# Kernel optimization log

Hardware: AMD Instinct MI355X
Metric: run time of the kernel (lower is better)

Reference implementation:

```python
import jax, jax.numpy as jnp
import numpy as np

B, S, D = 4, 1024, 1024
H, DK, DV = 16, 64, 64


def setup_inputs() -> dict:
    key = jax.random.key(0)
    ks = jax.random.split(key, 8)
    sc = 0.02
    return {
        "queries": jax.random.normal(ks[0], (B, S, D), jnp.float32),
        "keys": jax.random.normal(ks[1], (B, S, D), jnp.float32),
        "values": jax.random.normal(ks[2], (B, S, D), jnp.float32),
        "attn_bias": jax.random.normal(ks[3], (B, 1, S, S), jnp.float32),
        "Wq": jax.random.normal(ks[4], (H * DK, D), jnp.float32) * sc,
        "Wk": jax.random.normal(ks[5], (H * DK, D), jnp.float32) * sc,
        "Wv": jax.random.normal(ks[6], (H * DV, D), jnp.float32) * sc,
        "Wp": jax.random.normal(ks[7], (D, H * DV), jnp.float32) * sc,
    }


def reference(queries, keys, values, attn_bias, Wq, Wk, Wv, Wp):
    # Linear (no bias): x @ W.T, then split heads -> [B, H, S, d]
    q = (queries @ Wq.T).reshape(B, S, H, DK).transpose(0, 2, 1, 3)
    k = (keys @ Wk.T).reshape(B, S, H, DK).transpose(0, 2, 1, 3)
    v = (values @ Wv.T).reshape(B, S, H, DV).transpose(0, 2, 1, 3)
    # NOTE: original scales by d_model**-0.5, not d_key**-0.5
    scores = jnp.einsum("bhqd,bhkd->bhqk", q, k) * (D ** -0.5)
    scores = scores + attn_bias  # bias broadcasts over heads
    weights = jax.nn.softmax(scores, axis=-1)
    out = jnp.einsum("bhqk,bhkd->bhqd", weights, v)  # [B,H,S,DV]
    out = out.transpose(0, 2, 1, 3).reshape(B, S, H * DV)
    return out @ Wp.T
```

## Files before the change

### kernel.cpp

```cpp
#include <hip/hip_runtime.h>
#include <hip/hip_bf16.h>

typedef unsigned short u16;
typedef unsigned int u32;
typedef __attribute__((ext_vector_type(8))) short bf16x8;
typedef __attribute__((ext_vector_type(8))) u16 u16x8;
typedef __attribute__((ext_vector_type(4))) u16 u16x4;
typedef __attribute__((ext_vector_type(4))) u32 u32x4;
typedef __attribute__((ext_vector_type(4))) float f32x4;
typedef __attribute__((ext_vector_type(4))) _Float16 f16x4;
typedef __attribute__((ext_vector_type(8))) _Float16 f16x8;
typedef __attribute__((ext_vector_type(16))) float f32x16;

typedef const __attribute__((address_space(1))) void* gas1_t;
typedef __attribute__((address_space(3))) void* las3_t;

#define MFMA16(a,b,c) __builtin_amdgcn_mfma_f32_16x16x32_bf16((a),(b),(c),0,0,0)
#define MFMA32(a,b,c) __builtin_amdgcn_mfma_f32_32x32x16_bf16((a),(b),(c),0,0,0)

static constexpr int BB = 4, SS = 1024, DD = 1024, HH = 16;

static __device__ __forceinline__ u16 f2b(float x) {
  union { __hip_bfloat16 h; u16 u; } cv;
  cv.h = __float2bfloat16(x);
  return cv.u;
}
static __device__ __forceinline__ u32 pk2(float a, float b) {
  return (u32)f2b(a) | ((u32)f2b(b) << 16);
}

__global__ __launch_bounds__(256) void cvt_all(
    const float* __restrict__ q, const float* __restrict__ k, const float* __restrict__ v,
    const float* __restrict__ wq_, const float* __restrict__ wk_, const float* __restrict__ wv_,
    const float* __restrict__ wp_, const float* __restrict__ bias,
    u16* __restrict__ qb, u16* __restrict__ kb, u16* __restrict__ vb,
    u16* __restrict__ wqb, u16* __restrict__ wkb, u16* __restrict__ wvb, u16* __restrict__ wpb,
    _Float16* __restrict__ bias16) {
  int bid = blockIdx.x;
  if (bid >= 16384) {
    int G = (bid - 16384) * 256 + threadIdx.x;
    int gi = G & 1023;
    int ctid = gi & 255, g = gi >> 8;
    int T = G >> 10;
    int kt = T & 15, qt = (T >> 4) & 7, b_ = T >> 7;
    int wq = ctid >> 6, hi = (ctid >> 5) & 1, ln = ctid & 31;
    int qrow = qt * 128 + wq * 32 + ln;
    int kbf = g >> 1, j = g & 1;
    int k0 = kt * 64 + kbf * 32 + j * 16 + hi * 4;
    const float* src = bias + (((size_t)(b_ * 1024 + qrow)) << 10) + k0;
    float4 lo = *(const float4*)(src);
    float4 up = *(const float4*)(src + 8);
    f16x8 r = { (_Float16)lo.x, (_Float16)lo.y, (_Float16)lo.z, (_Float16)lo.w,
                (_Float16)up.x, (_Float16)up.y, (_Float16)up.z, (_Float16)up.w };
    *(f16x8*)(bias16 + (((size_t)T) << 13) + g * 2048 + ctid * 8) = r;
    return;
  }
  const float* s; u16* d; int off;
  if      (bid < 4096)  { s = q;   d = qb;  off = bid; }
  else if (bid < 8192)  { s = k;   d = kb;  off = bid - 4096; }
  else if (bid < 12288) { s = v;   d = vb;  off = bid - 8192; }
  else if (bid < 13312) { s = wq_; d = wqb; off = bid - 12288; }
  else if (bid < 14336) { s = wk_; d = wkb; off = bid - 13312; }
  else if (bid < 15360) { s = wv_; d = wvb; off = bid - 14336; }
  else                  { s = wp_; d = wpb; off = bid - 15360; }
  int i = (off * 256 + threadIdx.x) * 4;
  float4 val = *(const float4*)(s + i);
  u16x4 r = { f2b(val.x), f2b(val.y), f2b(val.z), f2b(val.w) };
  *(u16x4*)(d + i) = r;
}

template<typename OT, bool VTRANS>
__global__ __launch_bounds__(256) void gemm_bt(
    const u16* __restrict__ Abase, const u16* __restrict__ Wbase, OT* __restrict__ Cbase,
    u16* __restrict__ Tout, int N, int K, size_t sA, size_t sW, size_t sC) {
  const u16* A = Abase + (size_t)blockIdx.z * sA;
  const u16* W = Wbase + (size_t)blockIdx.z * sW;
  OT* C = Cbase + (size_t)blockIdx.z * sC;

  __shared__ __align__(16) u16 As[128 * 64];
  __shared__ __align__(16) u16 Bs[128 * 64];

  const int tid = threadIdx.x;
  const int lane = tid & 63;
  const int wid = tid >> 6;
  const int g = lane >> 4;
  const int li = lane & 15;

  const int hw = blockIdx.x + (blockIdx.y << 3);
  const int L = ((hw & 7) << 5) + (hw >> 3);
  const int brow = (L >> 3) * 128;
  const int bcol = (L & 7) * 128;

  const int wr = (wid >> 1) * 64;
  const int wc = (wid & 1) * 64;

  const int srow = wid * 8 + (lane >> 3);
  const int schunk = (lane & 7) ^ (lane >> 3);
  const u16* ga0 = A + (size_t)(brow + srow) * K + schunk * 8;
  const u16* gw0 = W + (size_t)(bcol + srow) * K + schunk * 8;

  f32x4 acc[4][4] = {};

  for (int k0 = 0; k0 < K; k0 += 64) {
#pragma unroll
    for (int i = 0; i < 4; ++i) {
      __builtin_amdgcn_global_load_lds((gas1_t)(const void*)(ga0 + (size_t)(i * 32) * K + k0),
                                       (las3_t)(void*)(As + (i * 32 + wid * 8) * 64), 16, 0, 0);
      __builtin_amdgcn_global_load_lds((gas1_t)(const void*)(gw0 + (size_t)(i * 32) * K + k0),
                                       (las3_t)(void*)(Bs + (i * 32 + wid * 8) * 64), 16, 0, 0);
    }
    __syncthreads();

#pragma unroll
    for (int kk = 0; kk < 2; ++kk) {
      bf16x8 a[4], b[4];
#pragma unroll
      for (int m = 0; m < 4; ++m) {
        int row = wr + m * 16 + li;
        a[m] = *(const bf16x8*)&As[row * 64 + (((kk * 4 + g) ^ (li & 7)) << 3)];
      }
#pragma unroll
      for (int n = 0; n < 4; ++n) {
        int row = wc + n * 16 + li;
        b[n] = *(const bf16x8*)&Bs[row * 64 + (((kk * 4 + g) ^ (li & 7)) << 3)];
      }
#pragma unroll
      for (int m = 0; m < 4; ++m)
#pragma unroll
        for (int n = 0; n < 4; ++n)
          acc[m][n] = MFMA16(a[m], b[n], acc[m][n]);
    }
    __syncthreads();
  }

  if (VTRANS && blockIdx.z == 2) {
#pragma unroll
    for (int m = 0; m < 4; ++m) {
#pragma unroll
      for (int n = 0; n < 4; ++n) {
        int c = bcol + wc + n * 16 + li;
        int h_ = c >> 6, dv = c & 63;
        int r0 = brow + wr + m * 16 + g * 4;
        int b_ = r0 >> 10, s0 = r0 & 1023;
        u16x4 val = { f2b(acc[m][n][0]), f2b(acc[m][n][1]),
                      f2b(acc[m][n][2]), f2b(acc[m][n][3]) };
        *(u16x4*)&Tout[(size_t)((b_ * HH + h_) * 64 + dv) * SS + s0] = val;
      }
    }
  } else {
#pragma unroll
    for (int m = 0; m < 4; ++m)
#pragma unroll
      for (int n = 0; n < 4; ++n)
#pragma unroll
        for (int j = 0; j < 4; ++j) {
          int r = brow + wr + m * 16 + g * 4 + j;
          int c = bcol + wc + n * 16 + li;
          if constexpr (sizeof(OT) == 2) C[(size_t)r * N + c] = (OT)f2b(acc[m][n][j]);
          else                           C[(size_t)r * N + c] = acc[m][n][j];
        }
  }
}

__global__ __launch_bounds__(512) void gemm_proj(
    const u16* __restrict__ A, const u16* __restrict__ W, float* __restrict__ C,
    int N, int K) {
  __shared__ __align__(16) u16 As[128 * 64];
  __shared__ __align__(16) u16 Bs[128 * 64];

  const int tid = threadIdx.x;
  const int lane = tid & 63;
  const int wid = tid >> 6;
  const int g = lane >> 4;
  const int li = lane & 15;

  const int hw = blockIdx.x + (blockIdx.y << 3);
  const int L = ((hw & 7) << 5) + (hw >> 3);
  const int brow = (L >> 3) * 128;
  const int bcol = (L & 7) * 128;

  const int wr = (wid >> 1) * 32;
  const int wc = (wid & 1) * 64;

  const int srow = tid >> 3;
  const int schunk = (tid & 7) ^ (srow & 7);
  const u16* ga0 = A + (size_t)(brow + srow) * K + schunk * 8;
  const u16* gw0 = W + (size_t)(bcol + srow) * K + schunk * 8;

  f32x4 acc[2][4] = {};

  for (int k0 = 0; k0 < K; k0 += 64) {
#pragma unroll
    for (int i = 0; i < 2; ++i) {
      __builtin_amdgcn_global_load_lds((gas1_t)(const void*)(ga0 + (size_t)(i * 64) * K + k0),
                                       (las3_t)(void*)(As + (i * 64 + (wid << 3)) * 64), 16, 0, 0);
      __builtin_amdgcn_global_load_lds((gas1_t)(const void*)(gw0 + (size_t)(i * 64) * K + k0),
                                       (las3_t)(void*)(Bs + (i * 64 + (wid << 3)) * 64), 16, 0, 0);
    }
    __syncthreads();

#pragma unroll
    for (int kk = 0; kk < 2; ++kk) {
      bf16x8 a[2], b[4];
#pragma unroll
      for (int m = 0; m < 2; ++m) {
        int row = wr + m * 16 + li;
        a[m] = *(const bf16x8*)&As[row * 64 + (((kk * 4 + g) ^ (li & 7)) << 3)];
      }
#pragma unroll
      for (int n = 0; n < 4; ++n) {
        int row = wc + n * 16 + li;
        b[n] = *(const bf16x8*)&Bs[row * 64 + (((kk * 4 + g) ^ (li & 7)) << 3)];
      }
#pragma unroll
      for (int m = 0; m < 2; ++m)
#pragma unroll
        for (int n = 0; n < 4; ++n)
          acc[m][n] = MFMA16(a[m], b[n], acc[m][n]);
    }
    __syncthreads();
  }

#pragma unroll
  for (int m = 0; m < 2; ++m)
#pragma unroll
    for (int n = 0; n < 4; ++n)
#pragma unroll
      for (int j = 0; j < 4; ++j) {
        int r = brow + wr + m * 16 + g * 4 + j;
        int c = bcol + wc + n * 16 + li;
        C[(size_t)r * N + c] = acc[m][n][j];
      }
}

__global__ __launch_bounds__(256) void attn_kernel(
    const u16* __restrict__ Q, const u16* __restrict__ K, const u16* __restrict__ Vt,
    const _Float16* __restrict__ bias16, u16* __restrict__ O) {
  __shared__ __align__(16) u16 kbuf[2][64 * 64];
  __shared__ __align__(16) u16 vbuf[2][64 * 64];

  const int tid = threadIdx.x;
  const int lane = tid & 63;
  const int wq = tid >> 6;
  const int hi = lane >> 5;
  const int ln = lane & 31;
  const u32 swz = (u32)(ln & 7) << 4;

  const int flat = blockIdx.x + (blockIdx.y << 3) + (blockIdx.z << 7);
  const int L = ((flat & 7) << 6) | (flat >> 3);
  const int qt = L & 7, h = (L >> 3) & 15, b = L >> 7;
  const int q0 = qt * 128;
  const int qrow = q0 + wq * 32 + ln;

  bf16x8 qf[4];
  {
    const u16* qp = Q + (size_t)(b * SS + qrow) * DD + h * 64 + hi * 8;
#pragma unroll
    for (int d = 0; d < 4; ++d) qf[d] = *(const bf16x8*)(qp + d * 16);
  }

  const int srow = (lane >> 3);
  const int spc = ((lane & 7) ^ srow) * 8;
  const u16* kgl = K + (size_t)(b * SS + wq * 16 + srow) * DD + h * 64 + spc;
  const u16* vgl = Vt + (size_t)((b * HH + h) * 64 + wq * 16 + srow) * SS + spc;

  const _Float16* btile = bias16 + (((size_t)(b * 8 + qt) * 16) << 13) + tid * 8;

  {
    char* kd = (char*)kbuf[0] + wq * 2048;
    char* vd = (char*)vbuf[0] + wq * 2048;
#pragma unroll
    for (int j = 0; j < 2; ++j) {
      __builtin_amdgcn_global_load_lds((gas1_t)(const void*)(kgl + (size_t)(j * 8) * DD),
                                       (las3_t)(void*)(kd + j * 1024), 16, 0, 0);
      __builtin_amdgcn_global_load_lds((gas1_t)(const void*)(vgl + (size_t)(j * 8) * SS),
                                       (las3_t)(void*)(vd + j * 1024), 16, 0, 0);
    }
  }
  f16x8 bbr[4], bbn[4];
#pragma unroll
  for (int g = 0; g < 4; ++g)
    bbr[g] = *(const f16x8*)(btile + g * 2048);
  __syncthreads();

  f32x16 o0 = {}, o1 = {};
  float m = -1e30f, lsum = 0.f;
  int cur = 0;

  for (int kt = 0; kt < 16; ++kt) {
    if (kt < 15) {
      char* kd = (char*)kbuf[cur ^ 1] + wq * 2048;
      char* vd = (char*)vbuf[cur ^ 1] + wq * 2048;
      const size_t k1 = (size_t)(kt + 1) * 64;
#pragma unroll
      for (int j = 0; j < 2; ++j) {
        __builtin_amdgcn_global_load_lds((gas1_t)(const void*)(kgl + (k1 + j * 8) * DD),
                                         (las3_t)(void*)(kd + j * 1024), 16, 0, 0);
        __builtin_amdgcn_global_load_lds((gas1_t)(const void*)(vgl + (size_t)(j * 8) * SS + k1),
                                         (las3_t)(void*)(vd + j * 1024), 16, 0, 0);
      }
      const _Float16* bt = btile + ((size_t)(kt + 1) << 13);
#pragma unroll
      for (int g = 0; g < 4; ++g)
        bbn[g] = *(const f16x8*)(bt + g * 2048);
    }

    const char* kb_base = (const char*)kbuf[cur];
    f32x16 s[2];
#pragma unroll
    for (int kb = 0; kb < 2; ++kb) {
      f32x16 acc = {};
#pragma unroll
      for (int d = 0; d < 4; ++d) {
        bf16x8 kf = *(const bf16x8*)(kb_base + (kb * 32 + ln) * 128 + (((u32)(d * 32 + hi * 16)) ^ swz));
        acc = MFMA32(kf, qf[d], acc);
      }
      s[kb] = acc;
    }

#pragma unroll
    for (int g = 0; g < 4; ++g) {
      const int kb = g >> 1, rq0 = (g & 1) * 2;
#pragma unroll
      for (int e = 0; e < 8; ++e)
        s[kb][(rq0 + (e >> 2)) * 4 + (e & 3)] =
            fmaf(s[kb][(rq0 + (e >> 2)) * 4 + (e & 3)], 0.03125f, (float)bbr[g][e]);
    }

    float mt = -1e30f;
#pragma unroll
    for (int r = 0; r < 16; ++r) { mt = fmaxf(mt, s[0][r]); mt = fmaxf(mt, s[1][r]); }
    mt = fmaxf(mt, __shfl_xor(mt, 32));

    bool resc = false;
    float fsc = 1.f;
    if (kt == 0) {
      m = mt;
    } else if (__any(mt > m + 8.f)) {
      float mn = fmaxf(m, mt);
      fsc = __expf(m - mn);
      m = mn;
      resc = true;
    }

    float rs = 0.f;
    u32 wv[2][8];
#pragma unroll
    for (int kb = 0; kb < 2; ++kb)
#pragma unroll
      for (int t = 0; t < 8; ++t) {
        float p0 = __expf(s[kb][2 * t] - m);
        float p1 = __expf(s[kb][2 * t + 1] - m);
        rs += p0 + p1;
        wv[kb][t] = pk2(p0, p1);
      }
    rs += __shfl_xor(rs, 32);
    lsum = lsum * fsc + rs;

    if (resc) {
#pragma unroll
      for (int j = 0; j < 16; ++j) {
        float fv = __shfl(fsc, (j & 3) + 8 * (j >> 2) + 4 * hi);
        o0[j] *= fv; o1[j] *= fv;
      }
    }

    const char* vb_base = (const char*)vbuf[cur];
#pragma unroll
    for (int ks = 0; ks < 4; ++ks) {
      const int kb = ks >> 1, i0 = (ks & 1) * 4;
      u32 sA = hi ? wv[kb][i0 + 0] : wv[kb][i0 + 2];
      u32 sB = hi ? wv[kb][i0 + 1] : wv[kb][i0 + 3];
      u32 rA = (u32)__shfl_xor((int)sA, 32);
      u32 rB = (u32)__shfl_xor((int)sB, 32);
      u32 e0 = hi ? rA : wv[kb][i0 + 0];
      u32 e1 = hi ? rB : wv[kb][i0 + 1];
      u32 e2 = hi ? wv[kb][i0 + 2] : rA;
      u32 e3 = hi ? wv[kb][i0 + 3] : rB;
      union { u32x4 u; bf16x8 v; } pc;
      pc.u = (u32x4){e0, e1, e2, e3};
      bf16x8 pa = pc.v;
#pragma unroll
      for (int nv = 0; nv < 2; ++nv) {
        bf16x8 vf = *(const bf16x8*)(vb_base + (nv * 32 + ln) * 128 + (((u32)(ks * 32 + hi * 16)) ^ swz));
        if (nv == 0) o0 = MFMA32(pa, vf, o0);
        else         o1 = MFMA32(pa, vf, o1);
      }
    }

    if (kt < 15) {
      __syncthreads();
      cur ^= 1;
#pragma unroll
      for (int g = 0; g < 4; ++g) bbr[g] = bbn[g];
    }
  }

  float inv = 1.0f / lsum;
#pragma unroll
  for (int j = 0; j < 16; ++j) {
    float iv = __shfl(inv, (j & 3) + 8 * (j >> 2) + 4 * hi);
    int q = q0 + wq * 32 + (j & 3) + 8 * (j >> 2) + 4 * hi;
    u16* op = O + (size_t)(b * SS + q) * DD + h * 64 + ln;
    op[0]  = f2b(o0[j] * iv);
    op[32] = f2b(o1[j] * iv);
  }
}

extern "C" void kernel_launch(void* const* d_in, const int* in_sizes, int n_in,
                              void* d_out, int out_size, void* d_ws, size_t ws_size,
                              hipStream_t stream) {
  const float* queries = (const float*)d_in[0];
  const float* keys    = (const float*)d_in[1];
  const float* values  = (const float*)d_in[2];
  const float* bias    = (const float*)d_in[3];
  const float* Wq      = (const float*)d_in[4];
  const float* Wk      = (const float*)d_in[5];
  const float* Wv      = (const float*)d_in[6];
  const float* Wp      = (const float*)d_in[7];
  float* out = (float*)d_out;

  char* ws = (char*)d_ws;
  const size_t MB = 1024 * 1024;
  u16* qb  = (u16*)(ws + 0 * MB);
  u16* kb  = (u16*)(ws + 8 * MB);
  u16* vb  = (u16*)(ws + 16 * MB);
  u16* wqb = (u16*)(ws + 24 * MB);
  u16* wkb = (u16*)(ws + 26 * MB);
  u16* wvb = (u16*)(ws + 28 * MB);
  u16* wpb = (u16*)(ws + 30 * MB);
  u16* Qb  = (u16*)(ws + 32 * MB);
  u16* Kb  = (u16*)(ws + 40 * MB);
  _Float16* bias16 = (_Float16*)(ws + 48 * MB);
  u16* Vtb = (u16*)(ws + 56 * MB);
  u16* Ob  = (u16*)(ws + 0 * MB);

  const int nAct = BB * SS * DD;
  const int nW = DD * DD;

  cvt_all<<<dim3(18432), dim3(256), 0, stream>>>(
      queries, keys, values, Wq, Wk, Wv, Wp, bias,
      qb, kb, vb, wqb, wkb, wvb, wpb, bias16);

  gemm_bt<u16, true><<<dim3(8, 32, 3), dim3(256), 0, stream>>>(
      qb, wqb, Qb, Vtb, DD, DD, (size_t)nAct, (size_t)nW, (size_t)nAct);

  attn_kernel<<<dim3(8, 16, 4), dim3(256), 0, stream>>>(Qb, Kb, Vtb, bias16, Ob);

  gemm_proj<<<dim3(8, 32), dim3(512), 0, stream>>>(Ob, wpb, out, DD, DD);
}
```

Measured before the change: 117.4 us.

## Double the attention key tile to 128 and load bias at iteration start

Result: slower. 125.8 us (+7.1%).

```diff
diff --git a/kernel.cpp b/kernel.cpp
--- a/kernel.cpp
+++ b/kernel.cpp
@@ -236,15 +236,16 @@
 __global__ __launch_bounds__(256) void attn_kernel(
     const u16* __restrict__ Q, const u16* __restrict__ K, const u16* __restrict__ Vt,
     const _Float16* __restrict__ bias16, u16* __restrict__ O) {
-  __shared__ __align__(16) u16 kbuf[2][64 * 64];
-  __shared__ __align__(16) u16 vbuf[2][64 * 64];
+  __shared__ __align__(16) u16 kbuf[2][128 * 64];
+  __shared__ __align__(16) u16 vbuf[2][64 * 128];
 
   const int tid = threadIdx.x;
   const int lane = tid & 63;
   const int wq = tid >> 6;
   const int hi = lane >> 5;
   const int ln = lane & 31;
-  const u32 swz = (u32)(ln & 7) << 4;
+  const u32 swzK = (u32)(ln & 7) << 4;
+  const u32 swzV = (u32)(ln & 15) << 4;
 
   const int flat = blockIdx.x + (blockIdx.y << 3) + (blockIdx.z << 7);
   const int L = ((flat & 7) << 6) | (flat >> 3);
@@ -259,77 +260,79 @@
     for (int d = 0; d < 4; ++d) qf[d] = *(const bf16x8*)(qp + d * 16);
   }
 
-  const int srow = (lane >> 3);
-  const int spc = ((lane & 7) ^ srow) * 8;
-  const u16* kgl = K + (size_t)(b * SS + wq * 16 + srow) * DD + h * 64 + spc;
-  const u16* vgl = Vt + (size_t)((b * HH + h) * 64 + wq * 16 + srow) * SS + spc;
+  const int sr8 = lane >> 3;
+  const int spcK = ((lane & 7) ^ sr8) * 8;
+  const u16* kgl = K + (size_t)(b * SS + wq * 32 + sr8) * DD + h * 64 + spcK;
+
+  const int vr4 = lane >> 4;
+  const u16* vgl = Vt + (size_t)((b * HH + h) * 64 + wq * 16 + vr4) * SS;
 
   const _Float16* btile = bias16 + (((size_t)(b * 8 + qt) * 16) << 13) + tid * 8;
 
-  {
-    char* kd = (char*)kbuf[0] + wq * 2048;
-    char* vd = (char*)vbuf[0] + wq * 2048;
-#pragma unroll
-    for (int j = 0; j < 2; ++j) {
-      __builtin_amdgcn_global_load_lds((gas1_t)(const void*)(kgl + (size_t)(j * 8) * DD),
-                                       (las3_t)(void*)(kd + j * 1024), 16, 0, 0);
-      __builtin_amdgcn_global_load_lds((gas1_t)(const void*)(vgl + (size_t)(j * 8) * SS),
-                                       (las3_t)(void*)(vd + j * 1024), 16, 0, 0);
-    }
-  }
-  f16x8 bbr[4], bbn[4];
-#pragma unroll
-  for (int g = 0; g < 4; ++g)
-    bbr[g] = *(const f16x8*)(btile + g * 2048);
+#define STAGE_KV(buf, ktv)                                                                 \
+  {                                                                                        \
+    char* kd = (char*)kbuf[buf] + wq * 4096;                                               \
+    char* vd = (char*)vbuf[buf] + wq * 4096;                                               \
+    _Pragma("unroll")                                                                      \
+    for (int j = 0; j < 4; ++j)                                                            \
+      __builtin_amdgcn_global_load_lds(                                                    \
+          (gas1_t)(const void*)(kgl + (size_t)((ktv) * 128 + j * 8) * DD),                 \
+          (las3_t)(void*)(kd + j * 1024), 16, 0, 0);                                       \
+    _Pragma("unroll")                                                                      \
+    for (int j = 0; j < 4; ++j)                                                            \
+      __builtin_amdgcn_global_load_lds(                                                    \
+          (gas1_t)(const void*)(vgl + (size_t)(j * 4) * SS + (ktv) * 128 +                 \
+                                ((lane & 15) ^ (j * 4 + vr4)) * 8),                        \
+          (las3_t)(void*)(vd + j * 1024), 16, 0, 0);                                       \
+  }
+
+  STAGE_KV(0, 0)
   __syncthreads();
 
   f32x16 o0 = {}, o1 = {};
   float m = -1e30f, lsum = 0.f;
   int cur = 0;
 
-  for (int kt = 0; kt < 16; ++kt) {
-    if (kt < 15) {
-      char* kd = (char*)kbuf[cur ^ 1] + wq * 2048;
-      char* vd = (char*)vbuf[cur ^ 1] + wq * 2048;
-      const size_t k1 = (size_t)(kt + 1) * 64;
-#pragma unroll
-      for (int j = 0; j < 2; ++j) {
-        __builtin_amdgcn_global_load_lds((gas1_t)(const void*)(kgl + (k1 + j * 8) * DD),
-                                         (las3_t)(void*)(kd + j * 1024), 16, 0, 0);
-        __builtin_amdgcn_global_load_lds((gas1_t)(const void*)(vgl + (size_t)(j * 8) * SS + k1),
-                                         (las3_t)(void*)(vd + j * 1024), 16, 0, 0);
-      }
-      const _Float16* bt = btile + ((size_t)(kt + 1) << 13);
-#pragma unroll
-      for (int g = 0; g < 4; ++g)
-        bbn[g] = *(const f16x8*)(bt + g * 2048);
-    }
+  for (int kt = 0; kt < 8; ++kt) {
+    f16x8 bbr[8];
+    {
+      const _Float16* bt = btile + ((size_t)(kt * 2) << 13);
+#pragma unroll
+      for (int g = 0; g < 4; ++g) bbr[g] = *(const f16x8*)(bt + g * 2048);
+#pragma unroll
+      for (int g = 0; g < 4; ++g) bbr[4 + g] = *(const f16x8*)(bt + 8192 + g * 2048);
+    }
+    if (kt < 7) STAGE_KV(cur ^ 1, kt + 1)
 
     const char* kb_base = (const char*)kbuf[cur];
-    f32x16 s[2];
-#pragma unroll
-    for (int kb = 0; kb < 2; ++kb) {
+    f32x16 s[4];
+#pragma unroll
+    for (int kbf = 0; kbf < 4; ++kbf) {
       f32x16 acc = {};
 #pragma unroll
       for (int d = 0; d < 4; ++d) {
-        bf16x8 kf = *(const bf16x8*)(kb_base + (kb * 32 + ln) * 128 + (((u32)(d * 32 + hi * 16)) ^ swz));
+        bf16x8 kf = *(const bf16x8*)(kb_base + (kbf * 32 + ln) * 128 + (((u32)(d * 32 + hi * 16)) ^ swzK));
         acc = MFMA32(kf, qf[d], acc);
       }
-      s[kb] = acc;
-    }
-
-#pragma unroll
-    for (int g = 0; g < 4; ++g) {
-      const int kb = g >> 1, rq0 = (g & 1) * 2;
+      s[kbf] = acc;
+    }
+
+#pragma unroll
+    for (int gp = 0; gp < 8; ++gp) {
+      const int kbf = ((gp >> 2) << 1) | ((gp >> 1) & 1), rq0 = (gp & 1) * 2;
 #pragma unroll
       for (int e = 0; e < 8; ++e)
-        s[kb][(rq0 + (e >> 2)) * 4 + (e & 3)] =
-            fmaf(s[kb][(rq0 + (e >> 2)) * 4 + (e & 3)], 0.03125f, (float)bbr[g][e]);
-    }
-
-    float mt = -1e30f;
-#pragma unroll
-    for (int r = 0; r < 16; ++r) { mt = fmaxf(mt, s[0][r]); mt = fmaxf(mt, s[1][r]); }
+        s[kbf][(rq0 + (e >> 2)) * 4 + (e & 3)] =
+            fmaf(s[kbf][(rq0 + (e >> 2)) * 4 + (e & 3)], 0.03125f, (float)bbr[gp][e]);
+    }
+
+    float r16[16];
+#pragma unroll
+    for (int i = 0; i < 16; ++i)
+      r16[i] = fmaxf(fmaxf(s[0][i], s[1][i]), fmaxf(s[2][i], s[3][i]));
+    float mt = r16[0];
+#pragma unroll
+    for (int i = 1; i < 16; ++i) mt = fmaxf(mt, r16[i]);
     mt = fmaxf(mt, __shfl_xor(mt, 32));
 
     bool resc = false;
@@ -344,15 +347,15 @@
     }
 
     float rs = 0.f;
-    u32 wv[2][8];
-#pragma unroll
-    for (int kb = 0; kb < 2; ++kb)
+    u32 wv[4][8];
+#pragma unroll
+    for (int kbf = 0; kbf < 4; ++kbf)
 #pragma unroll
       for (int t = 0; t < 8; ++t) {
-        float p0 = __expf(s[kb][2 * t] - m);
-        float p1 = __expf(s[kb][2 * t + 1] - m);
+        float p0 = __expf(s[kbf][2 * t] - m);
+        float p1 = __expf(s[kbf][2 * t + 1] - m);
         rs += p0 + p1;
-        wv[kb][t] = pk2(p0, p1);
+        wv[kbf][t] = pk2(p0, p1);
       }
     rs += __shfl_xor(rs, 32);
     lsum = lsum * fsc + rs;
@@ -367,34 +370,33 @@
 
     const char* vb_base = (const char*)vbuf[cur];
 #pragma unroll
-    for (int ks = 0; ks < 4; ++ks) {
-      const int kb = ks >> 1, i0 = (ks & 1) * 4;
-      u32 sA = hi ? wv[kb][i0 + 0] : wv[kb][i0 + 2];
-      u32 sB = hi ? wv[kb][i0 + 1] : wv[kb][i0 + 3];
+    for (int ks = 0; ks < 8; ++ks) {
+      const int kbf = ks >> 1, i0 = (ks & 1) * 4;
+      u32 sA = hi ? wv[kbf][i0 + 0] : wv[kbf][i0 + 2];
+      u32 sB = hi ? wv[kbf][i0 + 1] : wv[kbf][i0 + 3];
       u32 rA = (u32)__shfl_xor((int)sA, 32);
       u32 rB = (u32)__shfl_xor((int)sB, 32);
-      u32 e0 = hi ? rA : wv[kb][i0 + 0];
-      u32 e1 = hi ? rB : wv[kb][i0 + 1];
-      u32 e2 = hi ? wv[kb][i0 + 2] : rA;
-      u32 e3 = hi ? wv[kb][i0 + 3] : rB;
+      u32 e0 = hi ? rA : wv[kbf][i0 + 0];
+      u32 e1 = hi ? rB : wv[kbf][i0 + 1];
+      u32 e2 = hi ? wv[kbf][i0 + 2] : rA;
+      u32 e3 = hi ? wv[kbf][i0 + 3] : rB;
       union { u32x4 u; bf16x8 v; } pc;
       pc.u = (u32x4){e0, e1, e2, e3};
       bf16x8 pa = pc.v;
 #pragma unroll
       for (int nv = 0; nv < 2; ++nv) {
-        bf16x8 vf = *(const bf16x8*)(vb_base + (nv * 32 + ln) * 128 + (((u32)(ks * 32 + hi * 16)) ^ swz));
+        bf16x8 vf = *(const bf16x8*)(vb_base + (nv * 32 + ln) * 256 + (((u32)(ks * 32 + hi * 16)) ^ swzV));
         if (nv == 0) o0 = MFMA32(pa, vf, o0);
         else         o1 = MFMA32(pa, vf, o1);
       }
     }
 
-    if (kt < 15) {
+    if (kt < 7) {
       __syncthreads();
       cur ^= 1;
-#pragma unroll
-      for (int g = 0; g < 4; ++g) bbr[g] = bbn[g];
-    }
-  }
+    }
+  }
+#undef STAGE_KV
 
   float inv = 1.0f / lsum;
 #pragma unroll
```

## Fuse fp32-to-bf16 activation conversion into QKV projection GEMM

Applied to the files above, without the earlier changes.

Measured after the change: 112.4 us. -4.3%, faster.

```diff
diff --git a/kernel.cpp b/kernel.cpp
--- a/kernel.cpp
+++ b/kernel.cpp
@@ -28,17 +28,20 @@
 static __device__ __forceinline__ u32 pk2(float a, float b) {
   return (u32)f2b(a) | ((u32)f2b(b) << 16);
 }
+static __device__ __forceinline__ u32 cvtpk(float lo, float hi) {
+  u32 r;
+  asm("v_cvt_pk_bf16_f32 %0, %1, %2" : "=v"(r) : "v"(lo), "v"(hi));
+  return r;
+}
 
 __global__ __launch_bounds__(256) void cvt_all(
-    const float* __restrict__ q, const float* __restrict__ k, const float* __restrict__ v,
     const float* __restrict__ wq_, const float* __restrict__ wk_, const float* __restrict__ wv_,
     const float* __restrict__ wp_, const float* __restrict__ bias,
-    u16* __restrict__ qb, u16* __restrict__ kb, u16* __restrict__ vb,
     u16* __restrict__ wqb, u16* __restrict__ wkb, u16* __restrict__ wvb, u16* __restrict__ wpb,
     _Float16* __restrict__ bias16) {
   int bid = blockIdx.x;
-  if (bid >= 16384) {
-    int G = (bid - 16384) * 256 + threadIdx.x;
+  if (bid >= 4096) {
+    int G = (bid - 4096) * 256 + threadIdx.x;
     int gi = G & 1023;
     int ctid = gi & 255, g = gi >> 8;
     int T = G >> 10;
@@ -56,28 +59,25 @@
     return;
   }
   const float* s; u16* d; int off;
-  if      (bid < 4096)  { s = q;   d = qb;  off = bid; }
-  else if (bid < 8192)  { s = k;   d = kb;  off = bid - 4096; }
-  else if (bid < 12288) { s = v;   d = vb;  off = bid - 8192; }
-  else if (bid < 13312) { s = wq_; d = wqb; off = bid - 12288; }
-  else if (bid < 14336) { s = wk_; d = wkb; off = bid - 13312; }
-  else if (bid < 15360) { s = wv_; d = wvb; off = bid - 14336; }
-  else                  { s = wp_; d = wpb; off = bid - 15360; }
+  if      (bid < 1024) { s = wq_; d = wqb; off = bid; }
+  else if (bid < 2048) { s = wk_; d = wkb; off = bid - 1024; }
+  else if (bid < 3072) { s = wv_; d = wvb; off = bid - 2048; }
+  else                 { s = wp_; d = wpb; off = bid - 3072; }
   int i = (off * 256 + threadIdx.x) * 4;
   float4 val = *(const float4*)(s + i);
   u16x4 r = { f2b(val.x), f2b(val.y), f2b(val.z), f2b(val.w) };
   *(u16x4*)(d + i) = r;
 }
 
-template<typename OT, bool VTRANS>
-__global__ __launch_bounds__(256) void gemm_bt(
-    const u16* __restrict__ Abase, const u16* __restrict__ Wbase, OT* __restrict__ Cbase,
-    u16* __restrict__ Tout, int N, int K, size_t sA, size_t sW, size_t sC) {
-  const u16* A = Abase + (size_t)blockIdx.z * sA;
-  const u16* W = Wbase + (size_t)blockIdx.z * sW;
-  OT* C = Cbase + (size_t)blockIdx.z * sC;
-
-  __shared__ __align__(16) u16 As[128 * 64];
+__global__ __launch_bounds__(512) void gemm_qkv(
+    const float* __restrict__ Qf, const float* __restrict__ Kf, const float* __restrict__ Vf,
+    const u16* __restrict__ Wbase, u16* __restrict__ Qb, u16* __restrict__ Kb,
+    u16* __restrict__ Vtb) {
+  const int z = blockIdx.z;
+  const float* A = z == 0 ? Qf : (z == 1 ? Kf : Vf);
+  const u16* W = Wbase + (size_t)z * (DD * DD);
+
+  __shared__ __align__(16) float Af[128 * 64];
   __shared__ __align__(16) u16 Bs[128 * 64];
 
   const int tid = threadIdx.x;
@@ -91,33 +91,43 @@
   const int brow = (L >> 3) * 128;
   const int bcol = (L & 7) * 128;
 
-  const int wr = (wid >> 1) * 64;
+  const int wr = (wid >> 1) * 32;
   const int wc = (wid & 1) * 64;
 
-  const int srow = wid * 8 + (lane >> 3);
-  const int schunk = (lane & 7) ^ (lane >> 3);
-  const u16* ga0 = A + (size_t)(brow + srow) * K + schunk * 8;
-  const u16* gw0 = W + (size_t)(bcol + srow) * K + schunk * 8;
-
-  f32x4 acc[4][4] = {};
-
-  for (int k0 = 0; k0 < K; k0 += 64) {
-#pragma unroll
-    for (int i = 0; i < 4; ++i) {
-      __builtin_amdgcn_global_load_lds((gas1_t)(const void*)(ga0 + (size_t)(i * 32) * K + k0),
-                                       (las3_t)(void*)(As + (i * 32 + wid * 8) * 64), 16, 0, 0);
-      __builtin_amdgcn_global_load_lds((gas1_t)(const void*)(gw0 + (size_t)(i * 32) * K + k0),
-                                       (las3_t)(void*)(Bs + (i * 32 + wid * 8) * 64), 16, 0, 0);
-    }
+  const int arow = tid >> 4;
+  const int apc = (tid & 15) ^ (arow & 14);
+  const float* ga0 = A + (size_t)(brow + arow) * DD + apc * 4;
+
+  const int srw = tid >> 3;
+  const int spw = (tid & 7) ^ (srw & 7);
+  const u16* gw0 = W + (size_t)(bcol + srw) * DD + spw * 8;
+
+  f32x4 acc[2][4] = {};
+
+  for (int k0 = 0; k0 < DD; k0 += 64) {
+#pragma unroll
+    for (int i = 0; i < 4; ++i)
+      __builtin_amdgcn_global_load_lds((gas1_t)(const void*)(ga0 + (size_t)(i * 32) * DD + k0),
+                                       (las3_t)(void*)(Af + (i * 32 + (wid << 2)) * 64), 16, 0, 0);
+#pragma unroll
+    for (int i = 0; i < 2; ++i)
+      __builtin_amdgcn_global_load_lds((gas1_t)(const void*)(gw0 + (size_t)(i * 64) * DD + k0),
+                                       (las3_t)(void*)(Bs + (i * 64 + (wid << 3)) * 64), 16, 0, 0);
     __syncthreads();
 
 #pragma unroll
     for (int kk = 0; kk < 2; ++kk) {
-      bf16x8 a[4], b[4];
-#pragma unroll
-      for (int m = 0; m < 4; ++m) {
+      bf16x8 a[2], b[4];
+#pragma unroll
+      for (int m = 0; m < 2; ++m) {
         int row = wr + m * 16 + li;
-        a[m] = *(const bf16x8*)&As[row * 64 + (((kk * 4 + g) ^ (li & 7)) << 3)];
+        int gp = (2 * (kk * 4 + g)) ^ (li & 14);
+        f32x4 alo = *(const f32x4*)&Af[row * 64 + gp * 4];
+        f32x4 ahi = *(const f32x4*)&Af[row * 64 + (gp + 1) * 4];
+        union { u32x4 u; bf16x8 v; } ac;
+        ac.u = (u32x4){ cvtpk(alo[0], alo[1]), cvtpk(alo[2], alo[3]),
+                        cvtpk(ahi[0], ahi[1]), cvtpk(ahi[2], ahi[3]) };
+        a[m] = ac.v;
       }
 #pragma unroll
       for (int n = 0; n < 4; ++n) {
@@ -125,7 +135,7 @@
         b[n] = *(const bf16x8*)&Bs[row * 64 + (((kk * 4 + g) ^ (li & 7)) << 3)];
       }
 #pragma unroll
-      for (int m = 0; m < 4; ++m)
+      for (int m = 0; m < 2; ++m)
 #pragma unroll
         for (int n = 0; n < 4; ++n)
           acc[m][n] = MFMA16(a[m], b[n], acc[m][n]);
@@ -133,9 +143,9 @@
     __syncthreads();
   }
 
-  if (VTRANS && blockIdx.z == 2) {
-#pragma unroll
-    for (int m = 0; m < 4; ++m) {
+  if (z == 2) {
+#pragma unroll
+    for (int m = 0; m < 2; ++m) {
 #pragma unroll
       for (int n = 0; n < 4; ++n) {
         int c = bcol + wc + n * 16 + li;
@@ -144,20 +154,20 @@
         int b_ = r0 >> 10, s0 = r0 & 1023;
         u16x4 val = { f2b(acc[m][n][0]), f2b(acc[m][n][1]),
                       f2b(acc[m][n][2]), f2b(acc[m][n][3]) };
-        *(u16x4*)&Tout[(size_t)((b_ * HH + h_) * 64 + dv) * SS + s0] = val;
+        *(u16x4*)&Vtb[(size_t)((b_ * HH + h_) * 64 + dv) * SS + s0] = val;
       }
     }
   } else {
-#pragma unroll
-    for (int m = 0; m < 4; ++m)
+    u16* C = z == 0 ? Qb : Kb;
+#pragma unroll
+    for (int m = 0; m < 2; ++m)
 #pragma unroll
       for (int n = 0; n < 4; ++n)
 #pragma unroll
         for (int j = 0; j < 4; ++j) {
           int r = brow + wr + m * 16 + g * 4 + j;
           int c = bcol + wc + n * 16 + li;
-          if constexpr (sizeof(OT) == 2) C[(size_t)r * N + c] = (OT)f2b(acc[m][n][j]);
-          else                           C[(size_t)r * N + c] = acc[m][n][j];
+          C[(size_t)r * DD + c] = f2b(acc[m][n][j]);
         }
   }
 }
@@ -422,9 +432,6 @@
 
   char* ws = (char*)d_ws;
   const size_t MB = 1024 * 1024;
-  u16* qb  = (u16*)(ws + 0 * MB);
-  u16* kb  = (u16*)(ws + 8 * MB);
-  u16* vb  = (u16*)(ws + 16 * MB);
   u16* wqb = (u16*)(ws + 24 * MB);
   u16* wkb = (u16*)(ws + 26 * MB);
   u16* wvb = (u16*)(ws + 28 * MB);
@@ -435,17 +442,13 @@
   u16* Vtb = (u16*)(ws + 56 * MB);
   u16* Ob  = (u16*)(ws + 0 * MB);
 
-  const int nAct = BB * SS * DD;
-  const int nW = DD * DD;
-
-  cvt_all<<<dim3(18432), dim3(256), 0, stream>>>(
-      queries, keys, values, Wq, Wk, Wv, Wp, bias,
-      qb, kb, vb, wqb, wkb, wvb, wpb, bias16);
-
-  gemm_bt<u16, true><<<dim3(8, 32, 3), dim3(256), 0, stream>>>(
-      qb, wqb, Qb, Vtb, DD, DD, (size_t)nAct, (size_t)nW, (size_t)nAct);
+  cvt_all<<<dim3(6144), dim3(256), 0, stream>>>(
+      Wq, Wk, Wv, Wp, bias, wqb, wkb, wvb, wpb, bias16);
+
+  gemm_qkv<<<dim3(8, 32, 3), dim3(512), 0, stream>>>(
+      queries, keys, values, wqb, Qb, Kb, Vtb);
 
   attn_kernel<<<dim3(8, 16, 4), dim3(256), 0, stream>>>(Qb, Kb, Vtb, bias16, Ob);
 
-  gemm_proj<<<dim3(8, 32), dim3(512), 0, stream>>>(Ob, wpb, out, DD, DD);
-}
+  gemm_proj<<<dim3(8, 32, 1), dim3(512), 0, stream>>>(Ob, wpb, out, DD, DD);
+}
```
